# Optimization experiments

Measured on AMD Instinct MI355X. Metric: run time of the kernel, lower is better.

Reference implementation:

```python
import jax, jax.numpy as jnp
import numpy as np

HEADS = 8
DIM_HEAD = 64
MAX_POS = 512
SCALE = DIM_HEAD ** -0.5

def setup_inputs() -> dict:
    key = jax.random.key(0)
    ks = jax.random.split(key, 4)
    b, n, dim = 32, 512, 512
    x = jax.random.normal(ks[0], (b, n, dim), dtype=jnp.float32)
    W_qkv = jax.random.normal(ks[1], (dim, 3 * HEADS * DIM_HEAD), dtype=jnp.float32) * (dim ** -0.5)
    rel_table = jax.random.normal(ks[2], (2 * MAX_POS + 1, DIM_HEAD), dtype=jnp.float32) * 0.02
    W_out = jax.random.normal(ks[3], (HEADS * DIM_HEAD, dim), dtype=jnp.float32) * ((HEADS * DIM_HEAD) ** -0.5)
    b_out = jnp.zeros((dim,), dtype=jnp.float32)
    return {"x": x, "W_qkv": W_qkv, "rel_table": rel_table, "W_out": W_out, "b_out": b_out}

def reference(x, W_qkv, rel_table, W_out, b_out):
    b, n, dim = x.shape
    qkv = x @ W_qkv  # [b, n, 3*h*d]
    q, k, v = jnp.split(qkv, 3, axis=-1)
    def heads(t):  # [b, n, h*d] -> [b, h, n, d]
        return t.reshape(b, n, HEADS, DIM_HEAD).transpose(0, 2, 1, 3)
    q, k, v = heads(q), heads(k), heads(v)
    dots = jnp.einsum('bhid,bhjd->bhij', q, k) * SCALE
    # relative position bias
    seq = jnp.arange(n)
    dist = jnp.clip(seq[:, None] - seq[None, :], -MAX_POS, MAX_POS) + MAX_POS  # [n, n]
    rel = rel_table[dist]  # [n, n(=r), d]
    pos_attn = jnp.einsum('bhnd,nrd->bhnr', q, rel) * SCALE
    dots = dots + pos_attn
    attn = jax.nn.softmax(dots.astype(jnp.float32), axis=-1).astype(q.dtype)
    out = jnp.einsum('bhij,bhjd->bhid', attn, v)  # [b, h, n, d]
    out = out.transpose(0, 2, 1, 3).reshape(b, n, HEADS * DIM_HEAD)
    return out @ W_out + b_out  # dropout=0.0 -> identity
```

## Files before the change

### kernel.cpp

```cpp
#include <hip/hip_runtime.h>

typedef __attribute__((ext_vector_type(8))) short short8;
typedef __attribute__((ext_vector_type(4))) float floatx4;

static constexpr size_t QOFF = 0;
static constexpr size_t KOFF = 8388608;
static constexpr size_t VTOFF = 16777216;
static constexpr size_t RBOFF = 25165824;
static constexpr size_t XBOFF = 25231424;
static constexpr size_t WTOFF = 33620032;
static constexpr size_t WOTOFF = 34406464;
static constexpr size_t OBOFF = 34668608;

__device__ inline unsigned short f2b(float f) {
  unsigned int u = __float_as_uint(f);
  u += 0x7fffu + ((u >> 16) & 1u);
  return (unsigned short)(u >> 16);
}

__global__ void rel_cvt(const float* __restrict__ rel, unsigned short* __restrict__ dst) {
  int i = blockIdx.x * 256 + threadIdx.x;
  if (i < 65600) dst[i] = f2b(rel[i]);
}

__global__ __launch_bounds__(256) void x_cvt(const float* __restrict__ in,
                                             unsigned short* __restrict__ dst) {
  size_t i8 = ((size_t)blockIdx.x * 256 + threadIdx.x) * 8;
  float4 a = *(const float4*)(in + i8);
  float4 b = *(const float4*)(in + i8 + 4);
  unsigned short t[8] = {f2b(a.x), f2b(a.y), f2b(a.z), f2b(a.w),
                         f2b(b.x), f2b(b.y), f2b(b.z), f2b(b.w)};
  *(uint4*)(dst + i8) = *(uint4*)t;
}

__global__ __launch_bounds__(256) void t_cvt(const float* __restrict__ in,
                                             unsigned short* __restrict__ out,
                                             int R, int C) {
  __shared__ float T[64 * 65];
  const int tid = threadIdx.x;
  const int c0 = blockIdx.x * 64, r0 = blockIdx.y * 64;
#pragma unroll
  for (int p = 0; p < 4; ++p) {
    int r = (tid >> 4) + p * 16, c4 = (tid & 15) * 4;
    float4 v = *(const float4*)(in + (size_t)(r0 + r) * C + c0 + c4);
    T[r * 65 + c4 + 0] = v.x;
    T[r * 65 + c4 + 1] = v.y;
    T[r * 65 + c4 + 2] = v.z;
    T[r * 65 + c4 + 3] = v.w;
  }
  __syncthreads();
#pragma unroll
  for (int p = 0; p < 4; ++p) {
    int oc = (tid >> 4) + p * 16;
    int or4 = (tid & 15) * 4;
    unsigned short t[4];
#pragma unroll
    for (int j = 0; j < 4; ++j) t[j] = f2b(T[(or4 + j) * 65 + oc]);
    *(uint2*)(out + (size_t)(c0 + oc) * R + r0 + or4) = *(uint2*)t;
  }
}

__global__ __launch_bounds__(256) void qkv_mfma(const unsigned short* __restrict__ Xb,
                                                const unsigned short* __restrict__ Wt,
                                                unsigned short* __restrict__ wsb) {
  __shared__ __align__(16) unsigned short As[128 * 40];
  __shared__ __align__(16) unsigned short Bs[128 * 40];
  const int tid = threadIdx.x;
  const int w = tid >> 6, lane = tid & 63;
  const int g = lane >> 4, c = lane & 15;
  const int m0 = blockIdx.x * 128, n0 = blockIdx.y * 128;
  const int wr = (w >> 1) * 64, wc = (w & 1) * 64;
  const bool vmode = (blockIdx.y >= 8);

  floatx4 acc[4][4];
#pragma unroll
  for (int mi = 0; mi < 4; ++mi)
#pragma unroll
    for (int ni = 0; ni < 4; ++ni) acc[mi][ni] = (floatx4){0.f, 0.f, 0.f, 0.f};

  for (int kk = 0; kk < 512; kk += 32) {
    __syncthreads();
#pragma unroll
    for (int p = 0; p < 2; ++p) {
      int e = tid + 256 * p;
      int r = e >> 2, o = e & 3;
      *(uint4*)(As + r * 40 + o * 8) = *(const uint4*)(Xb + (size_t)(m0 + r) * 512 + kk + o * 8);
      *(uint4*)(Bs + r * 40 + o * 8) = *(const uint4*)(Wt + (size_t)(n0 + r) * 512 + kk + o * 8);
    }
    __syncthreads();
    short8 a[4], b[4];
#pragma unroll
    for (int mi = 0; mi < 4; ++mi) a[mi] = *(const short8*)(As + (wr + mi * 16 + c) * 40 + g * 8);
#pragma unroll
    for (int ni = 0; ni < 4; ++ni) b[ni] = *(const short8*)(Bs + (wc + ni * 16 + c) * 40 + g * 8);
    if (vmode) {
#pragma unroll
      for (int mi = 0; mi < 4; ++mi)
#pragma unroll
        for (int ni = 0; ni < 4; ++ni)
          acc[mi][ni] = __builtin_amdgcn_mfma_f32_16x16x32_bf16(b[ni], a[mi], acc[mi][ni], 0, 0, 0);
    } else {
#pragma unroll
      for (int mi = 0; mi < 4; ++mi)
#pragma unroll
        for (int ni = 0; ni < 4; ++ni)
          acc[mi][ni] = __builtin_amdgcn_mfma_f32_16x16x32_bf16(a[mi], b[ni], acc[mi][ni], 0, 0, 0);
    }
  }

  constexpr float SCL = 0.125f * 1.44269504088896340736f;
  if (vmode) {
#pragma unroll
    for (int mi = 0; mi < 4; ++mi) {
      const int xrow = m0 + wr + mi * 16 + c;
      const int bb = xrow >> 9, nn = xrow & 511;
#pragma unroll
      for (int ni = 0; ni < 4; ++ni) {
#pragma unroll
        for (int r = 0; r < 4; ++r) {
          const int C = n0 + wc + ni * 16 + g * 4 + r;
          const int col512 = C & 511;
          const int h = col512 >> 6, d = col512 & 63;
          wsb[VTOFF + (size_t)(bb * 8 + h) * 32768 + (size_t)d * 512 + nn] = f2b(acc[mi][ni][r]);
        }
      }
    }
  } else {
    const size_t base = (blockIdx.y >= 4) ? KOFF : QOFF;
    const float scl = (blockIdx.y >= 4) ? 1.0f : SCL;
#pragma unroll
    for (int ni = 0; ni < 4; ++ni) {
      const int C = n0 + wc + ni * 16 + c;
      const int col512 = C & 511;
      const int h = col512 >> 6, d = col512 & 63;
#pragma unroll
      for (int mi = 0; mi < 4; ++mi) {
#pragma unroll
        for (int r = 0; r < 4; ++r) {
          const int xrow = m0 + wr + mi * 16 + g * 4 + r;
          wsb[base + (size_t)((xrow >> 9) * 8 + h) * 32768 + (size_t)(xrow & 511) * 64 + d] =
              f2b(acc[mi][ni][r] * scl);
        }
      }
    }
  }
}

__global__ __launch_bounds__(256) void attn_mfma(const unsigned short* __restrict__ wsb,
                                                 unsigned short* __restrict__ Ob) {
  __shared__ __align__(16) unsigned short Ks[64 * 72];
  __shared__ __align__(16) unsigned short Vt[64 * 72];
  __shared__ __align__(16) unsigned short Ps[64 * 72];
  __shared__ __align__(16) float Gs[4 * 16 * 100];

  const int tid = threadIdx.x;
  const int w = tid >> 6, lane = tid & 63;
  const int g = lane >> 4, c = lane & 15;
  const int i0 = blockIdx.x * 64, bh = blockIdx.y;

  const unsigned short* Qg = wsb + QOFF + (size_t)bh * 32768 + (size_t)i0 * 64;
  const unsigned short* Kg = wsb + KOFF + (size_t)bh * 32768;
  const unsigned short* Vg = wsb + VTOFF + (size_t)bh * 32768;
  const unsigned short* Rg = wsb + RBOFF;

  const short8 bq0 = *(const short8*)(Qg + (size_t)(w * 16 + c) * 64 + g * 8);
  const short8 bq1 = *(const short8*)(Qg + (size_t)(w * 16 + c) * 64 + 32 + g * 8);

  float* GsW = Gs + w * 1600;
  unsigned short* PsW = Ps + (w * 16 + c) * 72;

  float m_i = -1e30f, l_i = 0.f;
  floatx4 oa[4];
#pragma unroll
  for (int t = 0; t < 4; ++t) oa[t] = (floatx4){0.f, 0.f, 0.f, 0.f};

  for (int jc = 0; jc < 8; ++jc) {
    const int j0 = jc * 64;
    __syncthreads();
    for (int e = tid; e < 512; e += 256) {
      int r = e >> 3, o = e & 7;
      *(uint4*)(Ks + r * 72 + o * 8) = *(const uint4*)(Kg + (size_t)(j0 + r) * 64 + o * 8);
      *(uint4*)(Vt + r * 72 + o * 8) = *(const uint4*)(Vg + (size_t)r * 512 + j0 + o * 8);
    }
    __syncthreads();

    const int dbase = i0 - j0 + 449 + w * 16;
    const unsigned short* Trow = Rg + (size_t)dbase * 64 + (size_t)c * 64;
#pragma unroll
    for (int dd = 0; dd < 6; ++dd) {
      short8 t0 = *(const short8*)(Trow + dd * 1024 + g * 8);
      short8 t1 = *(const short8*)(Trow + dd * 1024 + 32 + g * 8);
      floatx4 ga = (floatx4){0.f, 0.f, 0.f, 0.f};
      ga = __builtin_amdgcn_mfma_f32_16x16x32_bf16(t0, bq0, ga, 0, 0, 0);
      ga = __builtin_amdgcn_mfma_f32_16x16x32_bf16(t1, bq1, ga, 0, 0, 0);
      *(floatx4*)(GsW + c * 100 + dd * 16 + 4 * g) = ga;
    }

    floatx4 s4[4];
#pragma unroll
    for (int t = 0; t < 4; ++t) {
      short8 k0 = *(const short8*)(Ks + (t * 16 + c) * 72 + g * 8);
      short8 k1 = *(const short8*)(Ks + (t * 16 + c) * 72 + 32 + g * 8);
      floatx4 sa = (floatx4){0.f, 0.f, 0.f, 0.f};
      sa = __builtin_amdgcn_mfma_f32_16x16x32_bf16(k0, bq0, sa, 0, 0, 0);
      sa = __builtin_amdgcn_mfma_f32_16x16x32_bf16(k1, bq1, sa, 0, 0, 0);
      s4[t] = sa;
    }

    const float* Grow = GsW + c * 100 + c + 63;
#pragma unroll
    for (int t = 0; t < 4; ++t)
#pragma unroll
      for (int r = 0; r < 4; ++r) s4[t][r] += Grow[-(16 * t + 4 * g + r)];

    float mx = -1e30f;
#pragma unroll
    for (int t = 0; t < 4; ++t)
      mx = fmaxf(mx, fmaxf(fmaxf(s4[t][0], s4[t][1]), fmaxf(s4[t][2], s4[t][3])));
    mx = fmaxf(mx, __shfl_xor(mx, 16));
    mx = fmaxf(mx, __shfl_xor(mx, 32));
    const float mn = fmaxf(m_i, mx);
    const float al = exp2f(m_i - mn);
    m_i = mn;
    float ls = 0.f;
#pragma unroll
    for (int t = 0; t < 4; ++t)
#pragma unroll
      for (int r = 0; r < 4; ++r) {
        float p = exp2f(s4[t][r] - mn);
        s4[t][r] = p;
        ls += p;
      }
    ls += __shfl_xor(ls, 16);
    ls += __shfl_xor(ls, 32);
    l_i = l_i * al + ls;

#pragma unroll
    for (int r = 0; r < 4; ++r) {
      const float ar = __shfl(al, 4 * g + r);
#pragma unroll
      for (int dt = 0; dt < 4; ++dt) oa[dt][r] *= ar;
    }

#pragma unroll
    for (int t = 0; t < 4; ++t) {
      unsigned short pk[4] = {f2b(s4[t][0]), f2b(s4[t][1]), f2b(s4[t][2]), f2b(s4[t][3])};
      *(uint2*)(PsW + t * 16 + 4 * g) = *(uint2*)pk;
    }

    short8 ap0 = *(const short8*)(PsW + g * 8);
    short8 ap1 = *(const short8*)(PsW + 32 + g * 8);
#pragma unroll
    for (int dt = 0; dt < 4; ++dt) {
      short8 bv0 = *(const short8*)(Vt + (dt * 16 + c) * 72 + g * 8);
      short8 bv1 = *(const short8*)(Vt + (dt * 16 + c) * 72 + 32 + g * 8);
      oa[dt] = __builtin_amdgcn_mfma_f32_16x16x32_bf16(ap0, bv0, oa[dt], 0, 0, 0);
      oa[dt] = __builtin_amdgcn_mfma_f32_16x16x32_bf16(ap1, bv1, oa[dt], 0, 0, 0);
    }
  }

  const int b = bh >> 3, h = bh & 7;
  const float invl = 1.0f / l_i;
#pragma unroll
  for (int r = 0; r < 4; ++r) {
    const float inv = __shfl(invl, 4 * g + r);
    const int i = i0 + w * 16 + 4 * g + r;
    const size_t rowoff = ((size_t)(b * 512 + i)) * 512 + h * 64;
#pragma unroll
    for (int dt = 0; dt < 4; ++dt) Ob[rowoff + dt * 16 + c] = f2b(oa[dt][r] * inv);
  }
}

__global__ __launch_bounds__(256) void out_mfma(const unsigned short* __restrict__ Ab,
                                                const unsigned short* __restrict__ Bt,
                                                const float* __restrict__ bias,
                                                float* __restrict__ out) {
  __shared__ __align__(16) unsigned short As[128 * 40];
  __shared__ __align__(16) unsigned short Bs[128 * 40];
  const int tid = threadIdx.x;
  const int w = tid >> 6, lane = tid & 63;
  const int g = lane >> 4, c = lane & 15;
  const int m0 = blockIdx.x * 128, n0 = blockIdx.y * 128;
  const int wr = (w >> 1) * 64, wc = (w & 1) * 64;

  floatx4 acc[4][4];
#pragma unroll
  for (int mi = 0; mi < 4; ++mi)
#pragma unroll
    for (int ni = 0; ni < 4; ++ni) acc[mi][ni] = (floatx4){0.f, 0.f, 0.f, 0.f};

  for (int kk = 0; kk < 512; kk += 32) {
    __syncthreads();
#pragma unroll
    for (int p = 0; p < 2; ++p) {
      int e = tid + 256 * p;
      int r = e >> 2, o = e & 3;
      *(uint4*)(As + r * 40 + o * 8) = *(const uint4*)(Ab + (size_t)(m0 + r) * 512 + kk + o * 8);
      *(uint4*)(Bs + r * 40 + o * 8) = *(const uint4*)(Bt + (size_t)(n0 + r) * 512 + kk + o * 8);
    }
    __syncthreads();
    short8 a[4], b[4];
#pragma unroll
    for (int mi = 0; mi < 4; ++mi) a[mi] = *(const short8*)(As + (wr + mi * 16 + c) * 40 + g * 8);
#pragma unroll
    for (int ni = 0; ni < 4; ++ni) b[ni] = *(const short8*)(Bs + (wc + ni * 16 + c) * 40 + g * 8);
#pragma unroll
    for (int mi = 0; mi < 4; ++mi)
#pragma unroll
      for (int ni = 0; ni < 4; ++ni)
        acc[mi][ni] = __builtin_amdgcn_mfma_f32_16x16x32_bf16(a[mi], b[ni], acc[mi][ni], 0, 0, 0);
  }

#pragma unroll
  for (int ni = 0; ni < 4; ++ni) {
    const int C = n0 + wc + ni * 16 + c;
    const float bv = bias[C];
#pragma unroll
    for (int mi = 0; mi < 4; ++mi) {
#pragma unroll
      for (int r = 0; r < 4; ++r) {
        const int m = m0 + wr + mi * 16 + g * 4 + r;
        out[(size_t)m * 512 + C] = acc[mi][ni][r] + bv;
      }
    }
  }
}

extern "C" void kernel_launch(void* const* d_in, const int* in_sizes, int n_in,
                              void* d_out, int out_size, void* d_ws, size_t ws_size,
                              hipStream_t stream) {
  const float* x = (const float*)d_in[0];
  const float* Wqkv = (const float*)d_in[1];
  const float* rel = (const float*)d_in[2];
  const float* Wout = (const float*)d_in[3];
  const float* bout = (const float*)d_in[4];
  float* out = (float*)d_out;
  unsigned short* wsb = (unsigned short*)d_ws;

  rel_cvt<<<257, 256, 0, stream>>>(rel, wsb + RBOFF);
  x_cvt<<<4096, 256, 0, stream>>>(x, wsb + XBOFF);
  t_cvt<<<dim3(24, 8), 256, 0, stream>>>(Wqkv, wsb + WTOFF, 512, 1536);
  t_cvt<<<dim3(8, 8), 256, 0, stream>>>(Wout, wsb + WOTOFF, 512, 512);
  qkv_mfma<<<dim3(128, 12), 256, 0, stream>>>(wsb + XBOFF, wsb + WTOFF, wsb);
  attn_mfma<<<dim3(8, 256), 256, 0, stream>>>(wsb, wsb + OBOFF);
  out_mfma<<<dim3(128, 4), 256, 0, stream>>>(wsb + OBOFF, wsb + WOTOFF, bout, out);
}
```

Baseline: 305.1 us.

## Merge prep kernels, register-prefetch tiles in GEMM and attention, shrink bias LDS

The four conversion kernels are merged into one prep launch to cut launch overhead. The QKV GEMM and the attention kernel now prefetch the next K/V or A/B tile into registers while computing on the current one, so global load latency overlaps with MFMA work. In attention, the relative-position tiles are loaded early, the bias MFMA count drops from 6 to 5 slices, and the bias scratch in LDS is stored as bf16 instead of float. This lowers LDS footprint and may raise occupancy, but it adds register pressure and a small precision loss on the position bias.

```diff
diff --git a/kernel.cpp b/kernel.cpp
--- a/kernel.cpp
+++ b/kernel.cpp
@@ -17,46 +17,56 @@
   u += 0x7fffu + ((u >> 16) & 1u);
   return (unsigned short)(u >> 16);
 }
-
-__global__ void rel_cvt(const float* __restrict__ rel, unsigned short* __restrict__ dst) {
-  int i = blockIdx.x * 256 + threadIdx.x;
-  if (i < 65600) dst[i] = f2b(rel[i]);
-}
-
-__global__ __launch_bounds__(256) void x_cvt(const float* __restrict__ in,
-                                             unsigned short* __restrict__ dst) {
-  size_t i8 = ((size_t)blockIdx.x * 256 + threadIdx.x) * 8;
-  float4 a = *(const float4*)(in + i8);
-  float4 b = *(const float4*)(in + i8 + 4);
-  unsigned short t[8] = {f2b(a.x), f2b(a.y), f2b(a.z), f2b(a.w),
-                         f2b(b.x), f2b(b.y), f2b(b.z), f2b(b.w)};
-  *(uint4*)(dst + i8) = *(uint4*)t;
-}
-
-__global__ __launch_bounds__(256) void t_cvt(const float* __restrict__ in,
-                                             unsigned short* __restrict__ out,
-                                             int R, int C) {
+__device__ inline float b2f(unsigned short h) {
+  return __uint_as_float(((unsigned int)h) << 16);
+}
+
+__global__ __launch_bounds__(256) void prep(const float* __restrict__ x,
+                                            const float* __restrict__ Wqkv,
+                                            const float* __restrict__ Wout,
+                                            const float* __restrict__ rel,
+                                            unsigned short* __restrict__ wsb) {
   __shared__ float T[64 * 65];
+  const int bx = blockIdx.x;
   const int tid = threadIdx.x;
-  const int c0 = blockIdx.x * 64, r0 = blockIdx.y * 64;
-#pragma unroll
-  for (int p = 0; p < 4; ++p) {
-    int r = (tid >> 4) + p * 16, c4 = (tid & 15) * 4;
-    float4 v = *(const float4*)(in + (size_t)(r0 + r) * C + c0 + c4);
-    T[r * 65 + c4 + 0] = v.x;
-    T[r * 65 + c4 + 1] = v.y;
-    T[r * 65 + c4 + 2] = v.z;
-    T[r * 65 + c4 + 3] = v.w;
-  }
-  __syncthreads();
-#pragma unroll
-  for (int p = 0; p < 4; ++p) {
-    int oc = (tid >> 4) + p * 16;
-    int or4 = (tid & 15) * 4;
-    unsigned short t[4];
-#pragma unroll
-    for (int j = 0; j < 4; ++j) t[j] = f2b(T[(or4 + j) * 65 + oc]);
-    *(uint2*)(out + (size_t)(c0 + oc) * R + r0 + or4) = *(uint2*)t;
+  if (bx < 4096) {
+    size_t i8 = ((size_t)bx * 256 + tid) * 8;
+    float4 a = *(const float4*)(x + i8);
+    float4 b = *(const float4*)(x + i8 + 4);
+    unsigned short t[8] = {f2b(a.x), f2b(a.y), f2b(a.z), f2b(a.w),
+                           f2b(b.x), f2b(b.y), f2b(b.z), f2b(b.w)};
+    *(uint4*)(wsb + XBOFF + i8) = *(uint4*)t;
+  } else if (bx < 4352) {
+    const bool isq = bx < 4288;
+    const int z = isq ? bx - 4096 : bx - 4288;
+    const int C = isq ? 1536 : 512;
+    const int R = 512;
+    const int c0 = (isq ? (z % 24) : (z % 8)) * 64;
+    const int r0 = (isq ? (z / 24) : (z / 8)) * 64;
+    const float* in = isq ? Wqkv : Wout;
+    unsigned short* out = wsb + (isq ? WTOFF : WOTOFF);
+#pragma unroll
+    for (int p = 0; p < 4; ++p) {
+      int r = (tid >> 4) + p * 16, c4 = (tid & 15) * 4;
+      float4 v = *(const float4*)(in + (size_t)(r0 + r) * C + c0 + c4);
+      T[r * 65 + c4 + 0] = v.x;
+      T[r * 65 + c4 + 1] = v.y;
+      T[r * 65 + c4 + 2] = v.z;
+      T[r * 65 + c4 + 3] = v.w;
+    }
+    __syncthreads();
+#pragma unroll
+    for (int p = 0; p < 4; ++p) {
+      int oc = (tid >> 4) + p * 16;
+      int or4 = (tid & 15) * 4;
+      unsigned short t[4];
+#pragma unroll
+      for (int j = 0; j < 4; ++j) t[j] = f2b(T[(or4 + j) * 65 + oc]);
+      *(uint2*)(out + (size_t)(c0 + oc) * R + r0 + or4) = *(uint2*)t;
+    }
+  } else {
+    int i = (bx - 4352) * 256 + tid;
+    if (i < 65600) wsb[RBOFF + i] = f2b(rel[i]);
   }
 }
 
@@ -72,22 +82,32 @@
   const int wr = (w >> 1) * 64, wc = (w & 1) * 64;
   const bool vmode = (blockIdx.y >= 8);
 
+  const int rA = tid >> 2, oA = tid & 3;
+
   floatx4 acc[4][4];
 #pragma unroll
   for (int mi = 0; mi < 4; ++mi)
 #pragma unroll
     for (int ni = 0; ni < 4; ++ni) acc[mi][ni] = (floatx4){0.f, 0.f, 0.f, 0.f};
 
+  uint4 pa0 = *(const uint4*)(Xb + (size_t)(m0 + rA) * 512 + oA * 8);
+  uint4 pa1 = *(const uint4*)(Xb + (size_t)(m0 + rA + 64) * 512 + oA * 8);
+  uint4 pb0 = *(const uint4*)(Wt + (size_t)(n0 + rA) * 512 + oA * 8);
+  uint4 pb1 = *(const uint4*)(Wt + (size_t)(n0 + rA + 64) * 512 + oA * 8);
+
   for (int kk = 0; kk < 512; kk += 32) {
     __syncthreads();
-#pragma unroll
-    for (int p = 0; p < 2; ++p) {
-      int e = tid + 256 * p;
-      int r = e >> 2, o = e & 3;
-      *(uint4*)(As + r * 40 + o * 8) = *(const uint4*)(Xb + (size_t)(m0 + r) * 512 + kk + o * 8);
-      *(uint4*)(Bs + r * 40 + o * 8) = *(const uint4*)(Wt + (size_t)(n0 + r) * 512 + kk + o * 8);
-    }
-    __syncthreads();
+    *(uint4*)(As + rA * 40 + oA * 8) = pa0;
+    *(uint4*)(As + (rA + 64) * 40 + oA * 8) = pa1;
+    *(uint4*)(Bs + rA * 40 + oA * 8) = pb0;
+    *(uint4*)(Bs + (rA + 64) * 40 + oA * 8) = pb1;
+    __syncthreads();
+    const int kkn = (kk < 480) ? kk + 32 : kk;
+    pa0 = *(const uint4*)(Xb + (size_t)(m0 + rA) * 512 + kkn + oA * 8);
+    pa1 = *(const uint4*)(Xb + (size_t)(m0 + rA + 64) * 512 + kkn + oA * 8);
+    pb0 = *(const uint4*)(Wt + (size_t)(n0 + rA) * 512 + kkn + oA * 8);
+    pb1 = *(const uint4*)(Wt + (size_t)(n0 + rA + 64) * 512 + kkn + oA * 8);
+
     short8 a[4], b[4];
 #pragma unroll
     for (int mi = 0; mi < 4; ++mi) a[mi] = *(const short8*)(As + (wr + mi * 16 + c) * 40 + g * 8);
@@ -151,7 +171,7 @@
   __shared__ __align__(16) unsigned short Ks[64 * 72];
   __shared__ __align__(16) unsigned short Vt[64 * 72];
   __shared__ __align__(16) unsigned short Ps[64 * 72];
-  __shared__ __align__(16) float Gs[4 * 16 * 100];
+  __shared__ __align__(16) unsigned short Gs[4 * 16 * 84];
 
   const int tid = threadIdx.x;
   const int w = tid >> 6, lane = tid & 63;
@@ -166,8 +186,16 @@
   const short8 bq0 = *(const short8*)(Qg + (size_t)(w * 16 + c) * 64 + g * 8);
   const short8 bq1 = *(const short8*)(Qg + (size_t)(w * 16 + c) * 64 + 32 + g * 8);
 
-  float* GsW = Gs + w * 1600;
+  unsigned short* GsW = Gs + w * (16 * 84);
   unsigned short* PsW = Ps + (w * 16 + c) * 72;
+
+  const int r0s = tid >> 3, o0s = tid & 7;
+  const int r1s = r0s + 32;
+
+  uint4 pk0 = *(const uint4*)(Kg + (size_t)r0s * 64 + o0s * 8);
+  uint4 pk1 = *(const uint4*)(Kg + (size_t)r1s * 64 + o0s * 8);
+  uint4 pv0 = *(const uint4*)(Vg + (size_t)r0s * 512 + o0s * 8);
+  uint4 pv1 = *(const uint4*)(Vg + (size_t)r1s * 512 + o0s * 8);
 
   float m_i = -1e30f, l_i = 0.f;
   floatx4 oa[4];
@@ -177,24 +205,25 @@
   for (int jc = 0; jc < 8; ++jc) {
     const int j0 = jc * 64;
     __syncthreads();
-    for (int e = tid; e < 512; e += 256) {
-      int r = e >> 3, o = e & 7;
-      *(uint4*)(Ks + r * 72 + o * 8) = *(const uint4*)(Kg + (size_t)(j0 + r) * 64 + o * 8);
-      *(uint4*)(Vt + r * 72 + o * 8) = *(const uint4*)(Vg + (size_t)r * 512 + j0 + o * 8);
-    }
+    *(uint4*)(Ks + r0s * 72 + o0s * 8) = pk0;
+    *(uint4*)(Ks + r1s * 72 + o0s * 8) = pk1;
+    *(uint4*)(Vt + r0s * 72 + o0s * 8) = pv0;
+    *(uint4*)(Vt + r1s * 72 + o0s * 8) = pv1;
     __syncthreads();
 
     const int dbase = i0 - j0 + 449 + w * 16;
-    const unsigned short* Trow = Rg + (size_t)dbase * 64 + (size_t)c * 64;
-#pragma unroll
-    for (int dd = 0; dd < 6; ++dd) {
-      short8 t0 = *(const short8*)(Trow + dd * 1024 + g * 8);
-      short8 t1 = *(const short8*)(Trow + dd * 1024 + 32 + g * 8);
-      floatx4 ga = (floatx4){0.f, 0.f, 0.f, 0.f};
-      ga = __builtin_amdgcn_mfma_f32_16x16x32_bf16(t0, bq0, ga, 0, 0, 0);
-      ga = __builtin_amdgcn_mfma_f32_16x16x32_bf16(t1, bq1, ga, 0, 0, 0);
-      *(floatx4*)(GsW + c * 100 + dd * 16 + 4 * g) = ga;
-    }
+    const unsigned short* Trow = Rg + (size_t)(dbase + c) * 64;
+    short8 t0[5], t1[5];
+#pragma unroll
+    for (int dd = 0; dd < 5; ++dd) {
+      t0[dd] = *(const short8*)(Trow + dd * 1024 + g * 8);
+      t1[dd] = *(const short8*)(Trow + dd * 1024 + 32 + g * 8);
+    }
+    const int j0n = (jc < 7) ? j0 + 64 : j0;
+    pk0 = *(const uint4*)(Kg + (size_t)(j0n + r0s) * 64 + o0s * 8);
+    pk1 = *(const uint4*)(Kg + (size_t)(j0n + r1s) * 64 + o0s * 8);
+    pv0 = *(const uint4*)(Vg + (size_t)r0s * 512 + j0n + o0s * 8);
+    pv1 = *(const uint4*)(Vg + (size_t)r1s * 512 + j0n + o0s * 8);
 
     floatx4 s4[4];
 #pragma unroll
@@ -207,11 +236,20 @@
       s4[t] = sa;
     }
 
-    const float* Grow = GsW + c * 100 + c + 63;
+#pragma unroll
+    for (int dd = 0; dd < 5; ++dd) {
+      floatx4 ga = (floatx4){0.f, 0.f, 0.f, 0.f};
+      ga = __builtin_amdgcn_mfma_f32_16x16x32_bf16(t0[dd], bq0, ga, 0, 0, 0);
+      ga = __builtin_amdgcn_mfma_f32_16x16x32_bf16(t1[dd], bq1, ga, 0, 0, 0);
+      unsigned short gk[4] = {f2b(ga[0]), f2b(ga[1]), f2b(ga[2]), f2b(ga[3])};
+      *(uint2*)(GsW + c * 84 + dd * 16 + 4 * g) = *(uint2*)gk;
+    }
+
+    const unsigned short* Grow = GsW + c * 84 + c + 63;
 #pragma unroll
     for (int t = 0; t < 4; ++t)
 #pragma unroll
-      for (int r = 0; r < 4; ++r) s4[t][r] += Grow[-(16 * t + 4 * g + r)];
+      for (int r = 0; r < 4; ++r) s4[t][r] += b2f(Grow[-(16 * t + 4 * g + r)]);
 
     float mx = -1e30f;
 #pragma unroll
@@ -337,10 +375,7 @@
   float* out = (float*)d_out;
   unsigned short* wsb = (unsigned short*)d_ws;
 
-  rel_cvt<<<257, 256, 0, stream>>>(rel, wsb + RBOFF);
-  x_cvt<<<4096, 256, 0, stream>>>(x, wsb + XBOFF);
-  t_cvt<<<dim3(24, 8), 256, 0, stream>>>(Wqkv, wsb + WTOFF, 512, 1536);
-  t_cvt<<<dim3(8, 8), 256, 0, stream>>>(Wout, wsb + WOTOFF, 512, 512);
+  prep<<<4609, 256, 0, stream>>>(x, Wqkv, Wout, rel, wsb);
   qkv_mfma<<<dim3(128, 12), 256, 0, stream>>>(wsb + XBOFF, wsb + WTOFF, wsb);
   attn_mfma<<<dim3(8, 256), 256, 0, stream>>>(wsb, wsb + OBOFF);
   out_mfma<<<dim3(128, 4), 256, 0, stream>>>(wsb + OBOFF, wsb + WOTOFF, bout, out);
```

Result: faster. 247.0 us (-19.1%).
